# Optimization experiments

Measured on AMD Instinct MI355X. Metric: run time of the kernel, lower is better.

The kernel has to match this reference:

```python
import jax, jax.numpy as jnp
import numpy as np

B, C, H, W = 8, 512, 64, 64
CQ = C // 8  # query/key channels; must equal H==W for the mask broadcast to be valid


def _len_mask(n, length, dtype):
    keep = jnp.arange(n) < length
    return (keep[:, None] & keep[None, :]).astype(dtype)  # [n, n]


def setup_inputs() -> dict:
    key = jax.random.key(0)
    ks = jax.random.split(key, 10)
    s = lambda fan: 1.0 / np.sqrt(fan)
    return {
        "x1": jax.random.normal(ks[0], (B, C, H, W), jnp.float32),
        "x2": jax.random.normal(ks[1], (B, C, H, W), jnp.float32),
        "x3": jax.random.normal(ks[2], (B, C, H, W), jnp.float32),
        "Wq": jax.random.normal(ks[3], (CQ, C), jnp.float32) * s(C),
        "bq": jax.random.normal(ks[4], (CQ,), jnp.float32) * s(C),
        "Wk": jax.random.normal(ks[5], (CQ, C), jnp.float32) * s(C),
        "bk": jax.random.normal(ks[6], (CQ,), jnp.float32) * s(C),
        "Wv": jax.random.normal(ks[7], (C, C), jnp.float32) * s(C),
        "bv": jax.random.normal(ks[8], (C,), jnp.float32) * s(C),
        "gamma": jnp.asarray(0.5, jnp.float32),  # torch init is 0; nonzero to exercise the path
        "length": 32,
    }


def reference(x1, x2, x3, Wq, bq, Wk, bk, Wv, bv, gamma, length):
    b, c, h, w = x1.shape
    dt = x1.dtype
    # 1x1 convs as channel GEMMs
    q = jnp.einsum("bchw,oc->bohw", x1, Wq) + bq[None, :, None, None]  # [B,CQ,H,W]
    k = jnp.einsum("bchw,oc->bohw", x2, Wk) + bk[None, :, None, None]
    v = jnp.einsum("bchw,oc->bohw", x3, Wv) + bv[None, :, None, None]  # [B,C,H,W]

    mH = _len_mask(h, length, dt)  # [H,H] (CQ==H)
    mW = _len_mask(w, length, dt)  # [W,W] (CQ==W)

    # Column (H) attention branch
    qH = jnp.transpose(q, (0, 3, 2, 1)) * mH  # [B,W,H,CQ]
    kH = jnp.transpose(k, (0, 3, 1, 2)) * mH  # [B,W,CQ,H]
    eH = jnp.einsum("bwhc,bwcg->bwhg", qH, kH)  # [B,W,H,H]
    eH = jnp.where(jnp.eye(h, dtype=bool), -jnp.inf, eH)  # diagonal -inf trick
    eH = jnp.transpose(eH, (0, 2, 1, 3))  # [B,H,W,H]

    # Row (W) attention branch
    qW = jnp.transpose(q, (0, 2, 3, 1)) * mW  # [B,H,W,CQ]
    kW = jnp.transpose(k, (0, 2, 1, 3)) * mW  # [B,H,CQ,W]
    eW = jnp.einsum("bhwc,bhcg->bhwg", qW, kW)  # [B,H,W,W]

    att = jax.nn.softmax(jnp.concatenate([eH, eW], axis=3), axis=3)  # [B,H,W,H+W]
    attH = jnp.transpose(att[..., :h], (0, 2, 1, 3))  # [B,W,H,H]
    attW = att[..., h:]  # [B,H,W,W]

    vH = jnp.transpose(v, (0, 3, 1, 2))  # [B,W,C,H]
    vW = jnp.transpose(v, (0, 2, 1, 3))  # [B,H,C,W]
    outH = jnp.einsum("bwcj,bwij->bwci", vH, attH)  # [B,W,C,H]
    outH = jnp.transpose(outH, (0, 2, 3, 1))  # [B,C,H,W]
    outW = jnp.einsum("bhcj,bhij->bhci", vW, attW)  # [B,H,C,W]
    outW = jnp.transpose(outW, (0, 2, 1, 3))  # [B,C,H,W]

    return gamma * (outH + outW) + x1
```

## Files before the change

kernel.cpp:

```cpp
#include <hip/hip_runtime.h>
#include <math.h>
#include <type_traits>

#define CH 512
#define CQ 64
#define HH 64
#define WW 64
#define PP (HH*WW)
#define BB 8

typedef __bf16 bf16x8 __attribute__((ext_vector_type(8)));
typedef __bf16 bf16x4 __attribute__((ext_vector_type(4)));
typedef float  f32x4  __attribute__((ext_vector_type(4)));

__device__ __forceinline__ unsigned lds_off(const void* p) {
  return (unsigned)(size_t)(__attribute__((address_space(3))) const void*)p;
}
__device__ __forceinline__ bf16x4 ds_tr16(unsigned addr) {
  bf16x4 r;
  asm volatile("ds_read_b64_tr_b16 %0, %1" : "=v"(r) : "v"(addr));
  return r;
}

template<int FM, int FN, int NOUT, typename OutT>
__device__ __forceinline__ void proj_body(
    __bf16* AsBase, __bf16* BsBase,
    const float* __restrict__ X, const float* __restrict__ W,
    const float* __restrict__ bias, OutT* __restrict__ Y,
    int mblk, int nblk)
{
  constexpr int BM = 32 * FM;
  constexpr int BN = 32 * FN;
  constexpr int GA = BM / 64;
  constexpr int GB = BN / 64;
  typedef __bf16 (*TileA)[BM][40];
  typedef __bf16 (*TileB)[BN][40];
  TileA As = (TileA)AsBase;
  TileB Bs = (TileB)BsBase;

  const int tid = threadIdx.x;
  const int b     = mblk >> 12;
  const int pbase = mblk & 4095;
  const float* Xb = X + (size_t)b * CH * PP;

  const int l  = tid & 63;
  const int wv = tid >> 6;
  const int wr = wv >> 1, wc = wv & 1;
  const int lm = l & 15, lk = l >> 4;

  int ma[GA], ka[GA];
  #pragma unroll
  for (int gi = 0; gi < GA; ++gi) {
    int g = tid + gi * 256;
    ma[gi] = g % BM;
    ka[gi] = (g / BM) * 8;
  }
  int nb_[GB], kb_[GB];
  #pragma unroll
  for (int gi = 0; gi < GB; ++gi) {
    int g = tid + gi * 256;
    nb_[gi] = g >> 2;
    kb_[gi] = (g & 3) * 8;
  }

  float ra0[GA][8], ra1[GA][8];
  float rb[GB][8];

  auto loadA = [&](float (&ra)[GA][8], int c0) {
    #pragma unroll
    for (int gi = 0; gi < GA; ++gi)
      #pragma unroll
      for (int jj = 0; jj < 8; ++jj)
        ra[gi][jj] = Xb[(size_t)(c0 + ka[gi] + jj) * PP + pbase + ma[gi]];
  };
  auto loadB = [&](int c0) {
    #pragma unroll
    for (int gi = 0; gi < GB; ++gi) {
      const float* src = W + (size_t)(nblk + nb_[gi]) * CH + c0 + kb_[gi];
      float4 f0 = *(const float4*)src;
      float4 f1 = *(const float4*)(src + 4);
      rb[gi][0]=f0.x; rb[gi][1]=f0.y; rb[gi][2]=f0.z; rb[gi][3]=f0.w;
      rb[gi][4]=f1.x; rb[gi][5]=f1.y; rb[gi][6]=f1.z; rb[gi][7]=f1.w;
    }
  };

  f32x4 acc[FM][FN];
  #pragma unroll
  for (int j = 0; j < FN; ++j) {
    float bvj = bias[nblk + wc*FN*16 + j*16 + lm];
    #pragma unroll
    for (int i = 0; i < FM; ++i) {
      acc[i][j][0] = bvj; acc[i][j][1] = bvj;
      acc[i][j][2] = bvj; acc[i][j][3] = bvj;
    }
  }

  auto phase = [&](int t, auto par_c, float (&ra)[GA][8]) {
    constexpr int PAR = decltype(par_c)::value;
    #pragma unroll
    for (int gi = 0; gi < GA; ++gi) {
      bf16x8 hv;
      #pragma unroll
      for (int jj = 0; jj < 8; ++jj) hv[jj] = (__bf16)ra[gi][jj];
      *(bf16x8*)&As[PAR][ma[gi]][ka[gi]] = hv;
    }
    #pragma unroll
    for (int gi = 0; gi < GB; ++gi) {
      bf16x8 hv;
      #pragma unroll
      for (int jj = 0; jj < 8; ++jj) hv[jj] = (__bf16)rb[gi][jj];
      *(bf16x8*)&Bs[PAR][nb_[gi]][kb_[gi]] = hv;
    }
    __syncthreads();
    if (t < 15) loadB((t+1)*32);
    if (t < 14) loadA(ra, (t+2)*32);
    bf16x8 af[FM], bfr[FN];
    #pragma unroll
    for (int i = 0; i < FM; ++i)
      af[i] = *(const bf16x8*)&As[PAR][wr*FM*16 + i*16 + lm][lk*8];
    #pragma unroll
    for (int j = 0; j < FN; ++j)
      bfr[j] = *(const bf16x8*)&Bs[PAR][wc*FN*16 + j*16 + lm][lk*8];
    #pragma unroll
    for (int i = 0; i < FM; ++i)
      #pragma unroll
      for (int j = 0; j < FN; ++j)
        acc[i][j] = __builtin_amdgcn_mfma_f32_16x16x32_bf16(
            af[i], bfr[j], acc[i][j], 0, 0, 0);
  };

  loadA(ra0, 0); loadB(0); loadA(ra1, 32);
  for (int tt = 0; tt < 8; ++tt) {
    phase(2*tt,     std::integral_constant<int,0>{}, ra0);
    phase(2*tt + 1, std::integral_constant<int,1>{}, ra1);
  }

  #pragma unroll
  for (int i = 0; i < FM; ++i) {
    #pragma unroll
    for (int j = 0; j < FN; ++j) {
      #pragma unroll
      for (int r = 0; r < 4; ++r) {
        int mg = mblk + wr*FM*16 + i*16 + lk*4 + r;
        int ng = nblk + wc*FN*16 + j*16 + lm;
        Y[(size_t)mg * NOUT + ng] = (OutT)acc[i][j][r];
      }
    }
  }
}

__global__ __launch_bounds__(256) void proj_all_kernel(
    const float* __restrict__ x3, const float* __restrict__ Wv,
    const float* __restrict__ bv, __bf16* __restrict__ v_t,
    const float* __restrict__ x1, const float* __restrict__ Wq,
    const float* __restrict__ bq, float* __restrict__ q_t,
    const float* __restrict__ x2, const float* __restrict__ Wk,
    const float* __restrict__ bk, float* __restrict__ k_t)
{
  __shared__ __align__(16) __bf16 AsPool[2*128*40];
  __shared__ __align__(16) __bf16 BsPool[2*128*40];
  const int role = blockIdx.x;
  const int mblk = blockIdx.y * 128;
  if (role < 4) {
    proj_body<4,4, CH, __bf16>(AsPool, BsPool, x3, Wv, bv, v_t, mblk, role*128);
  } else if (role == 4) {
    proj_body<4,2, CQ, float >(AsPool, BsPool, x1, Wq, bq, q_t, mblk, 0);
  } else {
    proj_body<4,2, CQ, float >(AsPool, BsPool, x2, Wk, bk, k_t, mblk, 0);
  }
}

__global__ __launch_bounds__(256) void energyH_kernel(
    const float* __restrict__ qt, const float* __restrict__ kt,
    float* __restrict__ eH, const int* __restrict__ len_p)
{
  const int tid = threadIdx.x;
  const int w = blockIdx.x, b = blockIdx.y, zz = blockIdx.z;
  int L = *len_p; L = L < 0 ? 0 : (L > 64 ? 64 : L);
  __shared__ float Qs[32][68];
  __shared__ float Ks[64][68];
  {
    const int c = tid & 63, grp = tid >> 6;
    const float* qb = qt + ((size_t)b * PP + w) * CQ + c;
    const float* kb = kt + ((size_t)b * PP + w) * CQ + c;
    #pragma unroll
    for (int r = 0; r < 8; ++r) {
      int hl = grp*8 + r;
      Qs[hl][c] = qb[(size_t)(zz*32 + hl) * WW * CQ];
    }
    #pragma unroll
    for (int r = 0; r < 16; ++r) {
      int hk = grp*16 + r;
      Ks[hk][c] = kb[(size_t)hk * WW * CQ];
    }
  }
  __syncthreads();
  const int g  = tid & 63;
  const int wg = tid >> 6;
  float kreg[64];
  #pragma unroll
  for (int c = 0; c < 64; ++c) kreg[c] = (c < L) ? Ks[g][c] : 0.0f;
  const bool gok = (g < L);
  float* ab = eH + (((size_t)b * HH) * WW + w) * 64 + g;
  for (int r = 0; r < 8; ++r) {
    int hl = wg*8 + r;
    int h  = zz*32 + hl;
    float e = 0.0f;
    #pragma unroll
    for (int c4 = 0; c4 < 16; ++c4) {
      float4 q4 = *(const float4*)&Qs[hl][4*c4];
      e += q4.x*kreg[4*c4+0] + q4.y*kreg[4*c4+1]
         + q4.z*kreg[4*c4+2] + q4.w*kreg[4*c4+3];
    }
    e = (gok && h < L) ? e : 0.0f;
    if (g == h) e = -INFINITY;
    ab[(size_t)h * WW * 64] = e;
  }
}

__global__ __launch_bounds__(256) void energyW_softmax_kernel(
    const float* __restrict__ qt, const float* __restrict__ kt,
    const float* __restrict__ eH,
    __bf16* __restrict__ attHb, __bf16* __restrict__ attWb,
    const int* __restrict__ len_p)
{
  const int tid = threadIdx.x;
  const int h = blockIdx.x, b = blockIdx.y, zz = blockIdx.z;
  int L = *len_p; L = L < 0 ? 0 : (L > 64 ? 64 : L);
  __shared__ float Qs[32][68];
  __shared__ float Ks[64][68];
  {
    const int c = tid & 63, grp = tid >> 6;
    const float* qb = qt + ((size_t)b * PP + (size_t)h * WW) * CQ + c;
    const float* kb = kt + ((size_t)b * PP + (size_t)h * WW) * CQ + c;
    #pragma unroll
    for (int r = 0; r < 8; ++r) {
      int wl = grp*8 + r;
      Qs[wl][c] = qb[(size_t)(zz*32 + wl) * CQ];
    }
    #pragma unroll
    for (int r = 0; r < 16; ++r) {
      int wk = grp*16 + r;
      Ks[wk][c] = kb[(size_t)wk * CQ];
    }
  }
  __syncthreads();
  const int g  = tid & 63;
  const int wg = tid >> 6;
  float kreg[64];
  #pragma unroll
  for (int c = 0; c < 64; ++c) kreg[c] = (c < L) ? Ks[g][c] : 0.0f;
  const bool gok = (g < L);
  const float* ehb = eH + (((size_t)b * HH + h) * WW) * 64 + g;
  __bf16* ahb = attHb + (((size_t)b * HH + h) * WW) * 64 + g;
  __bf16* awb = attWb + (((size_t)b * HH + h) * WW) * 64 + g;
  for (int r = 0; r < 8; ++r) {
    int wl = wg*8 + r;
    int w  = zz*32 + wl;
    float e = 0.0f;
    #pragma unroll
    for (int c4 = 0; c4 < 16; ++c4) {
      float4 q4 = *(const float4*)&Qs[wl][4*c4];
      e += q4.x*kreg[4*c4+0] + q4.y*kreg[4*c4+1]
         + q4.z*kreg[4*c4+2] + q4.w*kreg[4*c4+3];
    }
    e = (gok && w < L) ? e : 0.0f;
    float eh = ehb[(size_t)w * 64];
    float m = fmaxf(e, eh);
    #pragma unroll
    for (int d = 32; d > 0; d >>= 1) m = fmaxf(m, __shfl_xor(m, d, 64));
    float pe = __expf(e  - m);
    float ph = __expf(eh - m);
    float s = pe + ph;
    #pragma unroll
    for (int d = 32; d > 0; d >>= 1) s += __shfl_xor(s, d, 64);
    float inv = 1.0f / s;
    ahb[(size_t)w * 64] = (__bf16)(ph * inv);
    awb[(size_t)w * 64] = (__bf16)(pe * inv);
  }
}

__device__ __forceinline__ int vsub64_off(int j, int c) {
  int s  = j >> 5;
  int p  = (j >> 2) & 1;
  int t  = ((j & 31) >> 3) * 4 + (j & 3);
  return ((s*2 + p)*4 + (c >> 4))*256 + t*16 + (c & 15);
}

__global__ __launch_bounds__(256) void outH_mfma_kernel(
    const __bf16* __restrict__ attHb, const __bf16* __restrict__ vt,
    __bf16* __restrict__ oH)
{
  const int tid = threadIdx.x;
  const int w = blockIdx.x, cq = blockIdx.y, b = blockIdx.z;
  const int l = tid & 63, wv = tid >> 6;
  const int lm = l & 15, lk = l >> 4;

  __shared__ __align__(16) __bf16 Bs[4096];

  #pragma unroll
  for (int i = 0; i < 2; ++i) {
    int j  = i*32 + (tid >> 3);
    int c0 = (tid & 7) * 8;
    bf16x8 v8 = *(const bf16x8*)(vt + ((size_t)b*PP + (size_t)j*WW + w)*CH + cq*64 + c0);
    *(bf16x8*)&Bs[vsub64_off(j, c0)] = v8;
  }

  const int hrow = wv*16 + lm;
  const __bf16* ab = attHb + (((size_t)b*HH + hrow)*WW + w)*64;
  bf16x8 af[2];
  af[0] = *(const bf16x8*)(ab + lk*8);
  af[1] = *(const bf16x8*)(ab + 32 + lk*8);
  __syncthreads();

  const unsigned bs_base = lds_off(&Bs[0]);
  f32x4 acc[4];
  #pragma unroll
  for (int f = 0; f < 4; ++f) acc[f] = (f32x4){0.f,0.f,0.f,0.f};
  #pragma unroll
  for (int s = 0; s < 2; ++s) {
    bf16x8 bfr[4];
    #pragma unroll
    for (int f = 0; f < 4; ++f) {
      unsigned base = bs_base + (unsigned)((((s*2)*4 + f)*512)) + (unsigned)(l*8);
      bf16x4 t0 = ds_tr16(base);
      bf16x4 t1 = ds_tr16(base + 2048);
      bfr[f] = __builtin_shufflevector(t0, t1, 0,1,2,3,4,5,6,7);
    }
    asm volatile("s_waitcnt lgkmcnt(0)");
    __builtin_amdgcn_sched_barrier(0);
    #pragma unroll
    for (int f = 0; f < 4; ++f)
      acc[f] = __builtin_amdgcn_mfma_f32_16x16x32_bf16(af[s], bfr[f], acc[f], 0,0,0);
  }
  __bf16* ob = oH + (((size_t)b * HH) * WW + w) * CH + cq*64;
  #pragma unroll
  for (int f = 0; f < 4; ++f) {
    #pragma unroll
    for (int r = 0; r < 4; ++r) {
      int h = wv*16 + lk*4 + r;
      ob[(size_t)h * WW * CH + f*16 + lm] = (__bf16)acc[f][r];
    }
  }
}

__global__ __launch_bounds__(256) void outW_final_kernel(
    const __bf16* __restrict__ attWb, const __bf16* __restrict__ vt,
    const __bf16* __restrict__ oH,
    const float* __restrict__ x1, const float* __restrict__ gamma_p,
    float* __restrict__ out)
{
  const int tid = threadIdx.x;
  const int h = blockIdx.x, cq = blockIdx.y, b = blockIdx.z;
  const int l = tid & 63, wv = tid >> 6;
  const int lm = l & 15, lk = l >> 4;
  const float gamma = *gamma_p;

  __shared__ __align__(16) char smem[64*69*4];
  __bf16* Bs = (__bf16*)smem;
  typedef float ScRow[69];
  ScRow* Sc = (ScRow*)smem;

  #pragma unroll
  for (int i = 0; i < 2; ++i) {
    int j  = i*32 + (tid >> 3);
    int c0 = (tid & 7) * 8;
    bf16x8 v8 = *(const bf16x8*)(vt + ((size_t)b*PP + (size_t)h*WW + j)*CH + cq*64 + c0);
    *(bf16x8*)&Bs[vsub64_off(j, c0)] = v8;
  }

  const int wrow = wv*16 + lm;
  const __bf16* ab = attWb + (((size_t)b*HH + h)*WW + wrow)*64;
  bf16x8 af[2];
  af[0] = *(const bf16x8*)(ab + lk*8);
  af[1] = *(const bf16x8*)(ab + 32 + lk*8);

  const int wl = tid & 63, cg = tid >> 6;
  const __bf16* ohb = oH + ((((size_t)b*HH + h) * WW) + wl) * CH + cq*64 + cg*16;
  bf16x8 ohr[2];
  ohr[0] = *(const bf16x8*)(ohb);
  ohr[1] = *(const bf16x8*)(ohb + 8);
  float x1r[16];
  {
    const float* x1b = x1 + ((size_t)b*CH + cq*64 + cg*16)*PP + (size_t)h*WW + wl;
    #pragma unroll
    for (int r2 = 0; r2 < 16; ++r2)
      x1r[r2] = x1b[(size_t)r2 * PP];
  }
  __syncthreads();

  const unsigned bs_base = lds_off(&Bs[0]);
  f32x4 acc[4];
  #pragma unroll
  for (int f = 0; f < 4; ++f) acc[f] = (f32x4){0.f,0.f,0.f,0.f};
  #pragma unroll
  for (int s = 0; s < 2; ++s) {
    bf16x8 bfr[4];
    #pragma unroll
    for (int f = 0; f < 4; ++f) {
      unsigned base = bs_base + (unsigned)((((s*2)*4 + f)*512)) + (unsigned)(l*8);
      bf16x4 t0 = ds_tr16(base);
      bf16x4 t1 = ds_tr16(base + 2048);
      bfr[f] = __builtin_shufflevector(t0, t1, 0,1,2,3,4,5,6,7);
    }
    asm volatile("s_waitcnt lgkmcnt(0)");
    __builtin_amdgcn_sched_barrier(0);
    #pragma unroll
    for (int f = 0; f < 4; ++f)
      acc[f] = __builtin_amdgcn_mfma_f32_16x16x32_bf16(af[s], bfr[f], acc[f], 0,0,0);
  }

  __syncthreads();
  #pragma unroll
  for (int f = 0; f < 4; ++f) {
    #pragma unroll
    for (int r = 0; r < 4; ++r)
      Sc[wv*16 + lk*4 + r][f*16 + lm] = acc[f][r];
  }
  __syncthreads();
  {
    float* obp = out + ((size_t)b*CH + cq*64 + cg*16)*PP + (size_t)h*WW + wl;
    #pragma unroll
    for (int r2 = 0; r2 < 16; ++r2) {
      float oh = (float)ohr[r2 >> 3][r2 & 7];
      obp[(size_t)r2 * PP] = gamma * (Sc[wl][cg*16 + r2] + oh) + x1r[r2];
    }
  }
}

extern "C" void kernel_launch(void* const* d_in, const int* in_sizes, int n_in,
                              void* d_out, int out_size, void* d_ws, size_t ws_size,
                              hipStream_t stream)
{
  const float* x1 = (const float*)d_in[0];
  const float* x2 = (const float*)d_in[1];
  const float* x3 = (const float*)d_in[2];
  const float* Wq = (const float*)d_in[3];
  const float* bq = (const float*)d_in[4];
  const float* Wk = (const float*)d_in[5];
  const float* bk = (const float*)d_in[6];
  const float* Wv = (const float*)d_in[7];
  const float* bv = (const float*)d_in[8];
  const float* gamma = (const float*)d_in[9];
  const int*   len   = (const int*)d_in[10];
  float* out = (float*)d_out;

  float*  q_t   = (float*)d_ws;
  float*  k_t   = q_t + (size_t)BB * PP * CQ;
  float*  eH    = k_t + (size_t)BB * PP * CQ;
  __bf16* attHb = (__bf16*)(eH + (size_t)BB * PP * 64);
  __bf16* attWb = attHb + (size_t)BB * PP * 64;
  __bf16* v_t   = attWb + (size_t)BB * PP * 64;
  __bf16* oH    = v_t + (size_t)BB * PP * CH;

  dim3 blk(256);
  proj_all_kernel<<<dim3(6, BB*PP/128), blk, 0, stream>>>(
      x3, Wv, bv, v_t,  x1, Wq, bq, q_t,  x2, Wk, bk, k_t);

  energyH_kernel<<<dim3(WW, BB, 2), blk, 0, stream>>>(q_t, k_t, eH, len);
  energyW_softmax_kernel<<<dim3(HH, BB, 2), blk, 0, stream>>>(q_t, k_t, eH, attHb, attWb, len);
  outH_mfma_kernel<<<dim3(WW, 8, BB), blk, 0, stream>>>(attHb, v_t, oH);
  outW_final_kernel<<<dim3(HH, 8, BB), blk, 0, stream>>>(attWb, v_t, oH, x1, gamma, out);
}
```

Baseline: 147.8 us.

## Vectorize projection A-tile loads with float4 and XOR-swizzled LDS layout

The activation tile loader in the projection GEMM now reads float4 vectors along the pixel dimension, four channels per thread, instead of scalar strided loads. It transposes them into bf16x4 LDS stores using an XOR swizzle on the k offset, and the fragment reads apply the matching swizzle to avoid bank conflicts. The launch grid is also transposed so that consecutive blocks walk over pixel tiles for a fixed role rather than over roles for a fixed tile, which changes L2 reuse of X and W. The swizzle must exactly match the reads for correctness, and the grid order change could reduce reuse of the shared x tile across the four Wv roles.

Result: faster. 144.2 us (-2.4%).

```diff
diff --git a/kernel.cpp b/kernel.cpp
--- a/kernel.cpp
+++ b/kernel.cpp
@@ -31,7 +31,6 @@
 {
   constexpr int BM = 32 * FM;
   constexpr int BN = 32 * FN;
-  constexpr int GA = BM / 64;
   constexpr int GB = BN / 64;
   typedef __bf16 (*TileA)[BM][40];
   typedef __bf16 (*TileB)[BN][40];
@@ -48,13 +47,11 @@
   const int wr = wv >> 1, wc = wv & 1;
   const int lm = l & 15, lk = l >> 4;
 
-  int ma[GA], ka[GA];
-  #pragma unroll
-  for (int gi = 0; gi < GA; ++gi) {
-    int g = tid + gi * 256;
-    ma[gi] = g % BM;
-    ka[gi] = (g / BM) * 8;
-  }
+  const int p4    = (tid & 31) * 4;
+  const int cbase = (tid >> 5) * 4;
+  const int uA    = ((cbase >> 3) ^ (tid & 3)) * 8 + ((cbase >> 2) & 1) * 4;
+  const int kfr   = (lk ^ (lm >> 2)) * 8;
+
   int nb_[GB], kb_[GB];
   #pragma unroll
   for (int gi = 0; gi < GB; ++gi) {
@@ -63,15 +60,14 @@
     kb_[gi] = (g & 3) * 8;
   }
 
-  float ra0[GA][8], ra1[GA][8];
+  float ra0[16], ra1[16];
   float rb[GB][8];
 
-  auto loadA = [&](float (&ra)[GA][8], int c0) {
-    #pragma unroll
-    for (int gi = 0; gi < GA; ++gi)
-      #pragma unroll
-      for (int jj = 0; jj < 8; ++jj)
-        ra[gi][jj] = Xb[(size_t)(c0 + ka[gi] + jj) * PP + pbase + ma[gi]];
+  auto loadA = [&](float (&ra)[16], int c0) {
+    #pragma unroll
+    for (int gi = 0; gi < 4; ++gi)
+      *(float4*)&ra[gi*4] =
+          *(const float4*)(Xb + (size_t)(c0 + cbase + gi) * PP + pbase + p4);
   };
   auto loadB = [&](int c0) {
     #pragma unroll
@@ -95,14 +91,16 @@
     }
   }
 
-  auto phase = [&](int t, auto par_c, float (&ra)[GA][8]) {
+  auto phase = [&](int t, auto par_c, float (&ra)[16]) {
     constexpr int PAR = decltype(par_c)::value;
     #pragma unroll
-    for (int gi = 0; gi < GA; ++gi) {
-      bf16x8 hv;
-      #pragma unroll
-      for (int jj = 0; jj < 8; ++jj) hv[jj] = (__bf16)ra[gi][jj];
-      *(bf16x8*)&As[PAR][ma[gi]][ka[gi]] = hv;
+    for (int pp = 0; pp < 4; ++pp) {
+      bf16x4 hv;
+      hv[0] = (__bf16)ra[0*4 + pp];
+      hv[1] = (__bf16)ra[1*4 + pp];
+      hv[2] = (__bf16)ra[2*4 + pp];
+      hv[3] = (__bf16)ra[3*4 + pp];
+      *(bf16x4*)&As[PAR][p4 + pp][uA] = hv;
     }
     #pragma unroll
     for (int gi = 0; gi < GB; ++gi) {
@@ -117,7 +115,7 @@
     bf16x8 af[FM], bfr[FN];
     #pragma unroll
     for (int i = 0; i < FM; ++i)
-      af[i] = *(const bf16x8*)&As[PAR][wr*FM*16 + i*16 + lm][lk*8];
+      af[i] = *(const bf16x8*)&As[PAR][wr*FM*16 + i*16 + lm][kfr];
     #pragma unroll
     for (int j = 0; j < FN; ++j)
       bfr[j] = *(const bf16x8*)&Bs[PAR][wc*FN*16 + j*16 + lm][lk*8];
@@ -159,8 +157,8 @@
 {
   __shared__ __align__(16) __bf16 AsPool[2*128*40];
   __shared__ __align__(16) __bf16 BsPool[2*128*40];
-  const int role = blockIdx.x;
-  const int mblk = blockIdx.y * 128;
+  const int role = blockIdx.y;
+  const int mblk = blockIdx.x * 128;
   if (role < 4) {
     proj_body<4,4, CH, __bf16>(AsPool, BsPool, x3, Wv, bv, v_t, mblk, role*128);
   } else if (role == 4) {
@@ -454,7 +452,7 @@
   __bf16* oH    = v_t + (size_t)BB * PP * CH;
 
   dim3 blk(256);
-  proj_all_kernel<<<dim3(6, BB*PP/128), blk, 0, stream>>>(
+  proj_all_kernel<<<dim3(BB*PP/128, 6), blk, 0, stream>>>(
       x3, Wv, bv, v_t,  x1, Wq, bq, q_t,  x2, Wk, bk, k_t);
 
   energyH_kernel<<<dim3(WW, BB, 2), blk, 0, stream>>>(q_t, k_t, eH, len);
```
